# Optimization experiments

Measured on AMD Instinct MI355X. Metric: run time of the kernel, lower is better.

## Reference

```python
import jax, jax.numpy as jnp
import numpy as np
import math

RADIUS = 0.2
NSAMPLE = 32
M = 8
EPS = 1e-6

def _normalize(v, axis):
    n = jnp.sqrt(jnp.sum(v * v, axis=axis, keepdims=True))
    return v / (n + EPS)

def _ball_query(xyz, new_xyz, fps_idx):
    # Emulates pointnet2 ball_query: first NSAMPLE in-radius indices in scan
    # order, padded with the first found index; rows with no hits stay 0.
    B, N, _ = xyz.shape
    d2 = jnp.sum((new_xyz[:, :, None, :] - xyz[:, None, :, :]) ** 2, axis=-1)  # (B,P,N)
    mask = d2 < RADIUS * RADIUS
    keys = jnp.where(mask, jnp.arange(N, dtype=jnp.int32)[None, None, :], N)
    neg_top, _ = jax.lax.top_k(-keys, NSAMPLE)
    sorted_idx = -neg_top  # ascending first NSAMPLE in-radius indices (or N pads)
    cnt = jnp.sum(mask, axis=-1, keepdims=True)
    first = jnp.where(cnt > 0, jnp.minimum(sorted_idx[..., :1], N - 1), 0)
    j = jnp.arange(NSAMPLE)[None, None, :]
    idx = jnp.where(j < cnt, sorted_idx, first).astype(jnp.int32)
    return jnp.concatenate([fps_idx[:, :, None].astype(jnp.int32), idx], axis=-1)  # (B,P,S+1)

def _group(features, idx):
    # features (B,C,N), idx (B,P,S) -> (B,C,P,S)
    return jax.vmap(lambda f, i: f[:, i])(features, idx)

def _project_one(p):
    # reference vector in plane orthogonal to normalized p; p (B,3,P,1)
    p = _normalize(p, 1)
    px, py, pz = p[:, 0], p[:, 1], p[:, 2]
    colin = jnp.abs(px) > 1.0 - 1e-3
    rx = jnp.where(colin, -py * px, 1.0 - px * px)
    ry = jnp.where(colin, 1.0 - py * py, -px * py)
    rz = jnp.where(colin, -py * pz, -px * pz)
    return _normalize(jnp.stack([rx, ry, rz], axis=1), 1)

def _rot_sort(p, pts):
    # sort pts (B,3,P,S) along S by clockwise angle of projection onto plane orthogonal to p
    p = _normalize(p, 1)
    ref = _project_one(p)
    vert = jnp.sum(p * pts, axis=1, keepdims=True) * p
    projs = _normalize(pts - vert, 1)
    refb = jnp.broadcast_to(ref, projs.shape)
    sinus = jnp.sum(jnp.cross(refb, projs, axis=1) * p, axis=1, keepdims=True)
    cosinus = jnp.sum(refb * projs, axis=1, keepdims=True)
    angles = jnp.arctan2(sinus, cosinus)  # (B,1,P,S)
    close = jnp.sum(projs * projs, axis=1, keepdims=True) < 1e-12
    rnd = (jax.random.uniform(jax.random.key(42), angles.shape) - 0.5) * (2.0 * math.pi)
    angles = jnp.where(close, rnd, angles)
    ind = jnp.argsort(angles, axis=-1)
    return jnp.take_along_axis(pts, jnp.broadcast_to(ind, pts.shape), axis=-1)

def _calc_invariance(center, rel):
    norm2 = jnp.sqrt(jnp.sum(rel * rel, axis=1, keepdims=True) + 1e-12)
    c = _normalize(center, 1)
    cosang = jnp.sum(c * rel, axis=1, keepdims=True) / norm2
    angle = jnp.arccos(jnp.clip(cosang, -1.0 + EPS, 1.0 - EPS))
    return jnp.concatenate([norm2, angle], axis=1)  # (B,2,P,S)

def _to_quat(xyz):
    dist = jnp.sqrt(jnp.sum(xyz * xyz, axis=1, keepdims=True))
    ori = xyz / (dist + EPS)
    theta = dist / RADIUS * (math.pi / 2.0)
    return jnp.concatenate([jnp.cos(theta), jnp.sin(theta) * ori], axis=1)  # (B,4,P,S)

def _forward(xyz, new_xyz, fps_idx):
    idx = _ball_query(xyz, new_xyz, fps_idx)                 # (B,P,S+1)
    grouped = _group(jnp.swapaxes(xyz, 1, 2), idx)           # (B,3,P,S+1)
    centers = jnp.swapaxes(new_xyz, 1, 2)[..., None]         # (B,3,P,1)
    grouped = _rot_sort(centers, grouped[..., 1:] - centers) # (B,3,P,S)
    inv = _calc_invariance(centers, grouped)                 # (B,2,P,S)
    q = _to_quat(grouped)                                    # (B,4,P,S)
    quats = jnp.stack([jnp.roll(q, -m, axis=-1) for m in range(M)], axis=2)  # (B,4,M,P,S)
    B, _, _, P, S = quats.shape
    quats = quats.reshape(B, 4 * M, P, S)
    return jnp.concatenate([inv, quats], axis=1)             # (B,34,P,S)

def setup_inputs() -> dict:
    key = jax.random.key(0)
    k1, k2 = jax.random.split(key)
    B, N, P = 4, 8192, 2048
    xyz = jax.random.uniform(k1, (B, N, 3), dtype=jnp.float32)
    fps_idx = jax.random.randint(k2, (B, P), 0, N, dtype=jnp.int32)
    new_xyz = jax.vmap(lambda x, i: x[i])(xyz, fps_idx)
    return {"xyz": xyz, "new_xyz": new_xyz, "fps_idx": fps_idx}

def reference(xyz, new_xyz, fps_idx):
    return _forward(xyz, new_xyz, fps_idx)
```

## Files before the change

### kernel.cpp

```cpp
#include <hip/hip_runtime.h>
#include <math.h>

constexpr int Bc  = 4;
constexpr int Nc  = 8192;
constexpr int Pc  = 2048;
constexpr int Sc  = 32;
constexpr int CHc = 34;
constexpr int WSTRIDE = 40;
constexpr int NQ  = Bc * Pc;
constexpr int SOA_OFF = NQ * WSTRIDE;
constexpr int BN      = Bc * Nc;

#define THREEFRY_PARTITIONABLE 1

#define FMUL __fmul_rn
#define FADD __fadd_rn
#define FSUB __fsub_rn

__device__ __forceinline__ unsigned tf_rotl(unsigned x, int r) {
  return (x << r) | (x >> (32 - r));
}

__device__ __forceinline__ void threefry2x32_k42(unsigned& x0, unsigned& x1) {
  const unsigned ks0 = 0u, ks1 = 42u, ks2 = 0u ^ 42u ^ 0x1BD11BDAu;
  x0 += ks0; x1 += ks1;
#define TF_ROUND(r) { x0 += x1; x1 = tf_rotl(x1, (r)); x1 ^= x0; }
  TF_ROUND(13) TF_ROUND(15) TF_ROUND(26) TF_ROUND(6)
  x0 += ks1; x1 += ks2 + 1u;
  TF_ROUND(17) TF_ROUND(29) TF_ROUND(16) TF_ROUND(24)
  x0 += ks2; x1 += ks0 + 2u;
  TF_ROUND(13) TF_ROUND(15) TF_ROUND(26) TF_ROUND(6)
  x0 += ks0; x1 += ks1 + 3u;
  TF_ROUND(17) TF_ROUND(29) TF_ROUND(16) TF_ROUND(24)
  x0 += ks1; x1 += ks2 + 4u;
  TF_ROUND(13) TF_ROUND(15) TF_ROUND(26) TF_ROUND(6)
  x0 += ks2; x1 += ks0 + 5u;
#undef TF_ROUND
}

__device__ __forceinline__ float jax_rnd_angle(unsigned n) {
#if THREEFRY_PARTITIONABLE
  unsigned x0 = 0u, x1 = n;
  threefry2x32_k42(x0, x1);
  unsigned bits = x0 ^ x1;
#else
  const unsigned half = (unsigned)(Bc * Pc * Sc) / 2u;
  unsigned x0, x1;
  bool second = (n >= half);
  if (second) { x0 = n - half; x1 = n; } else { x0 = n; x1 = n + half; }
  threefry2x32_k42(x0, x1);
  unsigned bits = second ? x1 : x0;
#endif
  float u = __uint_as_float((bits >> 9) | 0x3F800000u) - 1.0f;
  return FMUL(FSUB(u, 0.5f), (float)(2.0 * 3.141592653589793));
}

__device__ __forceinline__ float dot3rn(float ax, float ay, float az,
                                        float bx, float by, float bz) {
  return FADD(FADD(FMUL(ax, bx), FMUL(ay, by)), FMUL(az, bz));
}

__global__ __launch_bounds__(256)
void soa_kernel(const float* __restrict__ xyz, float* __restrict__ wsf)
{
  const int i = blockIdx.x * 256 + threadIdx.x;
  if (i < BN) {
    wsf[SOA_OFF + 0 * BN + i] = xyz[i * 3 + 0];
    wsf[SOA_OFF + 1 * BN + i] = xyz[i * 3 + 1];
    wsf[SOA_OFF + 2 * BN + i] = xyz[i * 3 + 2];
  }
}

__global__ __launch_bounds__(256)
void ball_kernel(const float* __restrict__ wsf,
                 const float* __restrict__ new_xyz,
                 int* __restrict__ ws)
{
  const int wave = threadIdx.x >> 6;
  const int lane = threadIdx.x & 63;
  const int q    = blockIdx.x * 4 + wave;
  const int b    = q >> 11;
  const int p    = q & 2047;

  const float* sxb = wsf + SOA_OFF + 0 * BN + b * Nc;
  const float* syb = wsf + SOA_OFF + 1 * BN + b * Nc;
  const float* szb = wsf + SOA_OFF + 2 * BN + b * Nc;

  const float cx = new_xyz[((size_t)b * Pc + p) * 3 + 0];
  const float cy = new_xyz[((size_t)b * Pc + p) * 3 + 1];
  const float cz = new_xyz[((size_t)b * Pc + p) * 3 + 2];

  int* wq = ws + (size_t)q * WSTRIDE;
  const float R2 = (float)(0.2 * 0.2);
  const unsigned long long below = (1ull << lane) - 1ull;

  auto loadw = [&](int basew, float xs[8], float ys[8], float zs[8]) {
    #pragma unroll
    for (int k = 0; k < 8; ++k) {
      const int i = basew + k * 64 + lane;
      xs[k] = sxb[i];
      ys[k] = syb[i];
      zs[k] = szb[i];
    }
  };
  auto procw = [&](int basew, const float xs[8], const float ys[8],
                   const float zs[8], int& run) {
    #pragma unroll
    for (int k = 0; k < 8; ++k) {
      const float dx = FSUB(cx, xs[k]);
      const float dy = FSUB(cy, ys[k]);
      const float dz = FSUB(cz, zs[k]);
      const float d2 = FADD(FADD(FMUL(dx, dx), FMUL(dy, dy)), FMUL(dz, dz));
      const bool m = d2 < R2;
      const unsigned long long mask = __ballot(m);
      if (m) {
        const int pos = run + (int)__popcll(mask & below);
        if (pos < Sc) wq[pos] = basew + k * 64 + lane;
      }
      run += (int)__popcll(mask);
    }
  };

  float ax[8], ay[8], az[8], bx[8], by[8], bz[8];
  loadw(0, ax, ay, az);
  int run = 0;
  #pragma unroll 1
  for (int basew = 0; basew < Nc; basew += 1024) {
    loadw(basew + 512, bx, by, bz);
    procw(basew, ax, ay, az, run);
    if (run >= Sc) break;
    loadw((basew + 1024) & (Nc - 1), ax, ay, az);
    procw(basew + 512, bx, by, bz, run);
    if (run >= Sc) break;
  }
  if (lane == 0) wq[Sc] = (run > Sc) ? Sc : run;
}

__global__ __launch_bounds__(256)
void emit_kernel(const float* __restrict__ xyz,
                 const float* __restrict__ new_xyz,
                 const int* __restrict__ ws,
                 float* __restrict__ out)
{
  const int wave = threadIdx.x >> 6;
  const int lane = threadIdx.x & 63;
  const int half = lane >> 5;
  const int hofs = half << 5;
  const int j    = lane & 31;
  const int q    = blockIdx.x * 8 + wave * 2 + half;
  const int b    = q >> 11;
  const int p    = q & 2047;

  const float* xb = xyz + (size_t)b * Nc * 3;
  const float cx = new_xyz[((size_t)b * Pc + p) * 3 + 0];
  const float cy = new_xyz[((size_t)b * Pc + p) * 3 + 1];
  const float cz = new_xyz[((size_t)b * Pc + p) * 3 + 2];

  const int* wq = ws + (size_t)q * WSTRIDE;
  const int cnt = wq[Sc];

  const int gi = wq[(j < cnt) ? j : 0];

  const float ptx = xb[gi * 3 + 0];
  const float pty = xb[gi * 3 + 1];
  const float ptz = xb[gi * 3 + 2];
  const float relx = FSUB(ptx, cx);
  const float rely = FSUB(pty, cy);
  const float relz = FSUB(ptz, cz);

  const float n1  = __fsqrt_rn(dot3rn(cx, cy, cz, cx, cy, cz));
  const float id1 = FADD(n1, 1e-6f);
  const float p1x = __fdiv_rn(cx, id1);
  const float p1y = __fdiv_rn(cy, id1);
  const float p1z = __fdiv_rn(cz, id1);

  const float n2  = __fsqrt_rn(dot3rn(p1x, p1y, p1z, p1x, p1y, p1z));
  const float id2 = FADD(n2, 1e-6f);
  const float p2x = __fdiv_rn(p1x, id2);
  const float p2y = __fdiv_rn(p1y, id2);
  const float p2z = __fdiv_rn(p1z, id2);

  const bool colin = fabsf(p2x) > (float)(1.0 - 0.001);
  const float rxv = colin ? FMUL(-p2y, p2x) : FSUB(1.0f, FMUL(p2x, p2x));
  const float ryv = colin ? FSUB(1.0f, FMUL(p2y, p2y)) : FMUL(-p2x, p2y);
  const float rzv = colin ? FMUL(-p2y, p2z) : FMUL(-p2x, p2z);
  const float nr  = __fsqrt_rn(dot3rn(rxv, ryv, rzv, rxv, ryv, rzv));
  const float idr = FADD(nr, 1e-6f);
  const float refx = __fdiv_rn(rxv, idr);
  const float refy = __fdiv_rn(ryv, idr);
  const float refz = __fdiv_rn(rzv, idr);

  const float sdot = dot3rn(p1x, p1y, p1z, relx, rely, relz);
  const float wx = FSUB(relx, FMUL(sdot, p1x));
  const float wy = FSUB(rely, FMUL(sdot, p1y));
  const float wz = FSUB(relz, FMUL(sdot, p1z));
  const float nw  = __fsqrt_rn(dot3rn(wx, wy, wz, wx, wy, wz));
  const float idw = FADD(nw, 1e-6f);
  const float prx = __fdiv_rn(wx, idw);
  const float pry = __fdiv_rn(wy, idw);
  const float prz = __fdiv_rn(wz, idw);

  const float s2 = dot3rn(prx, pry, prz, prx, pry, prz);

  float angle;
  if (s2 < 1e-12f) {
    const unsigned n = ((unsigned)q << 5) | (unsigned)j;
    angle = jax_rnd_angle(n);
  } else {
    const float ccx = FSUB(FMUL(refy, prz), FMUL(refz, pry));
    const float ccy = FSUB(FMUL(refz, prx), FMUL(refx, prz));
    const float ccz = FSUB(FMUL(refx, pry), FMUL(refy, prx));
    const float sinus   = dot3rn(ccx, ccy, ccz, p1x, p1y, p1z);
    const float cosinus = dot3rn(refx, refy, refz, prx, pry, prz);
    angle = atan2f(sinus, cosinus);
  }

  const unsigned ab   = __float_as_uint(angle);
  const unsigned skey = (ab & 0x80000000u) ? ~ab : (ab | 0x80000000u);
  unsigned long long key = ((unsigned long long)skey << 32) | (unsigned)j;

  #pragma unroll
  for (int k = 2; k <= 32; k <<= 1) {
    #pragma unroll
    for (int jj = k >> 1; jj > 0; jj >>= 1) {
      const unsigned long long other = __shfl_xor(key, jj);
      const bool up      = ((j & k) == 0);
      const bool lower   = ((j & jj) == 0);
      const bool takeMin = (lower == up);
      const unsigned long long mn = (key < other) ? key : other;
      const unsigned long long mx = (key < other) ? other : key;
      key = takeMin ? mn : mx;
    }
  }
  const int oj = (int)(key & 31u);

  const float sx = __shfl(relx, oj + hofs);
  const float sy = __shfl(rely, oj + hofs);
  const float sz = __shfl(relz, oj + hofs);

  const float dotr  = sx * sx + sy * sy + sz * sz;
  const float norm2 = sqrtf(dotr + 1e-12f);
  float cosang = (p1x * sx + p1y * sy + p1z * sz) / norm2;
  const float CL = (float)(1.0 - 1e-6);
  cosang = fminf(fmaxf(cosang, -CL), CL);
  const float ainv = acosf(cosang);

  const float dist = sqrtf(dotr);
  const float invd = 1.0f / (dist + 1e-6f);
  const float oxv = sx * invd, oyv = sy * invd, ozv = sz * invd;
  const float theta = (dist / 0.2f) * (float)(3.141592653589793 / 2.0);
  float st, ct;
  sincosf(theta, &st, &ct);
  const float qw = ct, qx = st * oxv, qy = st * oyv, qz = st * ozv;

  const size_t chs   = (size_t)Pc * Sc;
  const size_t baseo = (size_t)b * CHc * chs + (size_t)p * Sc + (size_t)j;

  out[baseo + 0 * chs] = norm2;
  out[baseo + 1 * chs] = ainv;
  #pragma unroll
  for (int m = 0; m < 8; ++m) {
    const int src = ((j + m) & 31) + hofs;
    const float vw = __shfl(qw, src);
    const float vx = __shfl(qx, src);
    const float vy = __shfl(qy, src);
    const float vz = __shfl(qz, src);
    out[baseo + (size_t)(2 + 0 * 8 + m) * chs] = vw;
    out[baseo + (size_t)(2 + 1 * 8 + m) * chs] = vx;
    out[baseo + (size_t)(2 + 2 * 8 + m) * chs] = vy;
    out[baseo + (size_t)(2 + 3 * 8 + m) * chs] = vz;
  }
}

extern "C" void kernel_launch(void* const* d_in, const int* in_sizes, int n_in,
                              void* d_out, int out_size, void* d_ws, size_t ws_size,
                              hipStream_t stream) {
  const float* xyz     = (const float*)d_in[0];
  const float* new_xyz = (const float*)d_in[1];
  float* out = (float*)d_out;
  int*   ws  = (int*)d_ws;
  float* wsf = (float*)d_ws;

  hipLaunchKernelGGL(soa_kernel, dim3((BN + 255) / 256), dim3(256), 0, stream,
                     xyz, wsf);

  hipLaunchKernelGGL(ball_kernel, dim3(NQ / 4), dim3(256), 0, stream,
                     wsf, new_xyz, ws);

  hipLaunchKernelGGL(emit_kernel, dim3(NQ / 8), dim3(256), 0, stream,
                     xyz, new_xyz, ws, out);
}
```

Measured before the change: 87.04 us.

## Share LDS-staged point windows across 16 queries per block in ball query

The ball-query kernel now has each block handle 16 query centers (4 per wave). Point coordinates are staged cooperatively into double-buffered LDS windows of 512 points, so each point load is reused across four centers per wave and sixteen per block. Hit indices are gathered in LDS and written out at the end, and the block exits early only when all waves are done. This cuts global/L2 traffic per query, but adds a block-wide barrier per window, and a block can now keep scanning past the point where a single query would have stopped.

Result: slower. 109.5 us (+25.8%).

```diff
diff --git a/kernel.cpp b/kernel.cpp
--- a/kernel.cpp
+++ b/kernel.cpp
@@ -10,6 +10,7 @@
 constexpr int NQ  = Bc * Pc;
 constexpr int SOA_OFF = NQ * WSTRIDE;
 constexpr int BN      = Bc * Nc;
+constexpr int NWIN    = Nc / 512;
 
 #define THREEFRY_PARTITIONABLE 1
 
@@ -76,64 +77,94 @@
                  const float* __restrict__ new_xyz,
                  int* __restrict__ ws)
 {
-  const int wave = threadIdx.x >> 6;
-  const int lane = threadIdx.x & 63;
-  const int q    = blockIdx.x * 4 + wave;
-  const int b    = q >> 11;
-  const int p    = q & 2047;
+  __shared__ float sx[2][512], sy[2][512], sz[2][512];
+  __shared__ int   sIdxL[16][Sc];
+  __shared__ int   sdone[4];
+
+  const int tid  = threadIdx.x;
+  const int wave = tid >> 6;
+  const int lane = tid & 63;
+  const int q0    = blockIdx.x * 16;
+  const int qbase = q0 + wave * 4;
+  const int b     = q0 >> 11;
 
   const float* sxb = wsf + SOA_OFF + 0 * BN + b * Nc;
   const float* syb = wsf + SOA_OFF + 1 * BN + b * Nc;
   const float* szb = wsf + SOA_OFF + 2 * BN + b * Nc;
 
-  const float cx = new_xyz[((size_t)b * Pc + p) * 3 + 0];
-  const float cy = new_xyz[((size_t)b * Pc + p) * 3 + 1];
-  const float cz = new_xyz[((size_t)b * Pc + p) * 3 + 2];
-
-  int* wq = ws + (size_t)q * WSTRIDE;
+  float cx[4], cy[4], cz[4];
+  #pragma unroll
+  for (int i = 0; i < 4; ++i) {
+    const int p = (qbase + i) & 2047;
+    cx[i] = new_xyz[((size_t)b * Pc + p) * 3 + 0];
+    cy[i] = new_xyz[((size_t)b * Pc + p) * 3 + 1];
+    cz[i] = new_xyz[((size_t)b * Pc + p) * 3 + 2];
+  }
+
   const float R2 = (float)(0.2 * 0.2);
   const unsigned long long below = (1ull << lane) - 1ull;
 
-  auto loadw = [&](int basew, float xs[8], float ys[8], float zs[8]) {
-    #pragma unroll
-    for (int k = 0; k < 8; ++k) {
-      const int i = basew + k * 64 + lane;
-      xs[k] = sxb[i];
-      ys[k] = syb[i];
-      zs[k] = szb[i];
+  auto stage = [&](int wnd, int buf) {
+    const int basep = wnd * 512;
+    sx[buf][tid]       = sxb[basep + tid];
+    sy[buf][tid]       = syb[basep + tid];
+    sz[buf][tid]       = szb[basep + tid];
+    sx[buf][tid + 256] = sxb[basep + tid + 256];
+    sy[buf][tid + 256] = syb[basep + tid + 256];
+    sz[buf][tid + 256] = szb[basep + tid + 256];
+  };
+
+  int run4[4] = {0, 0, 0, 0};
+
+  auto procwin = [&](int wnd, int buf) {
+    #pragma unroll 1
+    for (int g = 0; g < 8; ++g) {
+      const float px = sx[buf][g * 64 + lane];
+      const float py = sy[buf][g * 64 + lane];
+      const float pz = sz[buf][g * 64 + lane];
+      #pragma unroll
+      for (int i = 0; i < 4; ++i) {
+        const float dx = FSUB(cx[i], px);
+        const float dy = FSUB(cy[i], py);
+        const float dz = FSUB(cz[i], pz);
+        const float d2 = FADD(FADD(FMUL(dx, dx), FMUL(dy, dy)), FMUL(dz, dz));
+        const bool m = d2 < R2;
+        const unsigned long long mask = __ballot(m);
+        if (m) {
+          const int pos = run4[i] + (int)__popcll(mask & below);
+          if (pos < Sc) sIdxL[wave * 4 + i][pos] = wnd * 512 + g * 64 + lane;
+        }
+        run4[i] += (int)__popcll(mask);
+      }
     }
   };
-  auto procw = [&](int basew, const float xs[8], const float ys[8],
-                   const float zs[8], int& run) {
-    #pragma unroll
-    for (int k = 0; k < 8; ++k) {
-      const float dx = FSUB(cx, xs[k]);
-      const float dy = FSUB(cy, ys[k]);
-      const float dz = FSUB(cz, zs[k]);
-      const float d2 = FADD(FADD(FMUL(dx, dx), FMUL(dy, dy)), FMUL(dz, dz));
-      const bool m = d2 < R2;
-      const unsigned long long mask = __ballot(m);
-      if (m) {
-        const int pos = run + (int)__popcll(mask & below);
-        if (pos < Sc) wq[pos] = basew + k * 64 + lane;
-      }
-      run += (int)__popcll(mask);
+
+  if (tid < 4) sdone[tid] = 0;
+  stage(0, 0);
+  bool mydone = false;
+  int w = 0;
+  #pragma unroll 1
+  for (;;) {
+    __syncthreads();
+    if (w >= NWIN) break;
+    if ((sdone[0] & sdone[1] & sdone[2] & sdone[3]) != 0) break;
+    if (w + 1 < NWIN) stage(w + 1, (w + 1) & 1);
+    if (!mydone) {
+      procwin(w, w & 1);
+      mydone = (run4[0] >= Sc) & (run4[1] >= Sc) &
+               (run4[2] >= Sc) & (run4[3] >= Sc);
+      if (mydone && lane == 0) sdone[wave] = 1;
     }
-  };
-
-  float ax[8], ay[8], az[8], bx[8], by[8], bz[8];
-  loadw(0, ax, ay, az);
-  int run = 0;
-  #pragma unroll 1
-  for (int basew = 0; basew < Nc; basew += 1024) {
-    loadw(basew + 512, bx, by, bz);
-    procw(basew, ax, ay, az, run);
-    if (run >= Sc) break;
-    loadw((basew + 1024) & (Nc - 1), ax, ay, az);
-    procw(basew + 512, bx, by, bz, run);
-    if (run >= Sc) break;
-  }
-  if (lane == 0) wq[Sc] = (run > Sc) ? Sc : run;
+    ++w;
+  }
+
+  #pragma unroll
+  for (int i = 0; i < 4; ++i) {
+    int* wq = ws + (size_t)(qbase + i) * WSTRIDE;
+    const int cnt = (run4[i] > Sc) ? Sc : run4[i];
+    if (lane < Sc) wq[lane] = sIdxL[wave * 4 + i][lane];
+    if (lane == 0) wq[Sc] = cnt;
+  }
 }
 
 __global__ __launch_bounds__(256)
@@ -284,7 +315,7 @@
   hipLaunchKernelGGL(soa_kernel, dim3((BN + 255) / 256), dim3(256), 0, stream,
                      xyz, wsf);
 
-  hipLaunchKernelGGL(ball_kernel, dim3(NQ / 4), dim3(256), 0, stream,
+  hipLaunchKernelGGL(ball_kernel, dim3(NQ / 16), dim3(256), 0, stream,
                      wsf, new_xyz, ws);
 
   hipLaunchKernelGGL(emit_kernel, dim3(NQ / 8), dim3(256), 0, stream,
```

## Fuse SoA transpose, ball query and emit into one kernel with two queries per wave

Applied to the files above, without the earlier changes.

Merges the three kernels into one: each wave now handles two query centers, scanning the point cloud once and testing both against each loaded point. Neighbor indices go to LDS instead of a global workspace, and points are read directly from the AoS xyz array, so the SoA transpose kernel is dropped. This removes two launches and the workspace round-trip and halves the number of point loads per query. In exchange each wave keeps scanning until both queries are full, loads become strided AoS reads, and the scan and emit phases now share one block's occupancy.

New measurement: 84.50 us. -2.9%, faster.

```diff
diff --git a/kernel.cpp b/kernel.cpp
--- a/kernel.cpp
+++ b/kernel.cpp
@@ -1,15 +1,13 @@
 #include <hip/hip_runtime.h>
 #include <math.h>
+
 
 constexpr int Bc  = 4;
 constexpr int Nc  = 8192;
 constexpr int Pc  = 2048;
 constexpr int Sc  = 32;
 constexpr int CHc = 34;
-constexpr int WSTRIDE = 40;
 constexpr int NQ  = Bc * Pc;
-constexpr int SOA_OFF = NQ * WSTRIDE;
-constexpr int BN      = Bc * Nc;
 
 #define THREEFRY_PARTITIONABLE 1
 
@@ -61,36 +59,27 @@
 }
 
 __global__ __launch_bounds__(256)
-void soa_kernel(const float* __restrict__ xyz, float* __restrict__ wsf)
+void qgq_fused(const float* __restrict__ xyz,
+               const float* __restrict__ new_xyz,
+               float* __restrict__ out)
 {
-  const int i = blockIdx.x * 256 + threadIdx.x;
-  if (i < BN) {
-    wsf[SOA_OFF + 0 * BN + i] = xyz[i * 3 + 0];
-    wsf[SOA_OFF + 1 * BN + i] = xyz[i * 3 + 1];
-    wsf[SOA_OFF + 2 * BN + i] = xyz[i * 3 + 2];
-  }
-}
-
-__global__ __launch_bounds__(256)
-void ball_kernel(const float* __restrict__ wsf,
-                 const float* __restrict__ new_xyz,
-                 int* __restrict__ ws)
-{
+  __shared__ int sIdx[4][2 * Sc];
+
   const int wave = threadIdx.x >> 6;
   const int lane = threadIdx.x & 63;
-  const int q    = blockIdx.x * 4 + wave;
-  const int b    = q >> 11;
-  const int p    = q & 2047;
-
-  const float* sxb = wsf + SOA_OFF + 0 * BN + b * Nc;
-  const float* syb = wsf + SOA_OFF + 1 * BN + b * Nc;
-  const float* szb = wsf + SOA_OFF + 2 * BN + b * Nc;
-
-  const float cx = new_xyz[((size_t)b * Pc + p) * 3 + 0];
-  const float cy = new_xyz[((size_t)b * Pc + p) * 3 + 1];
-  const float cz = new_xyz[((size_t)b * Pc + p) * 3 + 2];
-
-  int* wq = ws + (size_t)q * WSTRIDE;
+  const int q0   = blockIdx.x * 8 + wave * 2;
+  const int b    = q0 >> 11;
+  const int p0   = q0 & 2047;
+
+  const float* xb = xyz + (size_t)b * Nc * 3;
+  const float c0x = new_xyz[((size_t)b * Pc + p0) * 3 + 0];
+  const float c0y = new_xyz[((size_t)b * Pc + p0) * 3 + 1];
+  const float c0z = new_xyz[((size_t)b * Pc + p0) * 3 + 2];
+  const float c1x = new_xyz[((size_t)b * Pc + p0 + 1) * 3 + 0];
+  const float c1y = new_xyz[((size_t)b * Pc + p0 + 1) * 3 + 1];
+  const float c1z = new_xyz[((size_t)b * Pc + p0 + 1) * 3 + 2];
+
+  int* sw = sIdx[wave];
   const float R2 = (float)(0.2 * 0.2);
   const unsigned long long below = (1ull << lane) - 1ull;
 
@@ -98,68 +87,73 @@
     #pragma unroll
     for (int k = 0; k < 8; ++k) {
       const int i = basew + k * 64 + lane;
-      xs[k] = sxb[i];
-      ys[k] = syb[i];
-      zs[k] = szb[i];
+      xs[k] = xb[i * 3 + 0];
+      ys[k] = xb[i * 3 + 1];
+      zs[k] = xb[i * 3 + 2];
     }
   };
+
+  int run0 = 0, run1 = 0;
   auto procw = [&](int basew, const float xs[8], const float ys[8],
-                   const float zs[8], int& run) {
+                   const float zs[8]) {
     #pragma unroll
     for (int k = 0; k < 8; ++k) {
-      const float dx = FSUB(cx, xs[k]);
-      const float dy = FSUB(cy, ys[k]);
-      const float dz = FSUB(cz, zs[k]);
-      const float d2 = FADD(FADD(FMUL(dx, dx), FMUL(dy, dy)), FMUL(dz, dz));
-      const bool m = d2 < R2;
-      const unsigned long long mask = __ballot(m);
-      if (m) {
-        const int pos = run + (int)__popcll(mask & below);
-        if (pos < Sc) wq[pos] = basew + k * 64 + lane;
+      const int idx = basew + k * 64 + lane;
+      {
+        const float dx = FSUB(c0x, xs[k]);
+        const float dy = FSUB(c0y, ys[k]);
+        const float dz = FSUB(c0z, zs[k]);
+        const float d2 = FADD(FADD(FMUL(dx, dx), FMUL(dy, dy)), FMUL(dz, dz));
+        const bool m = d2 < R2;
+        const unsigned long long mask = __ballot(m);
+        if (m) {
+          const int pos = run0 + (int)__popcll(mask & below);
+          if (pos < Sc) sw[pos] = idx;
+        }
+        run0 += (int)__popcll(mask);
       }
-      run += (int)__popcll(mask);
+      {
+        const float dx = FSUB(c1x, xs[k]);
+        const float dy = FSUB(c1y, ys[k]);
+        const float dz = FSUB(c1z, zs[k]);
+        const float d2 = FADD(FADD(FMUL(dx, dx), FMUL(dy, dy)), FMUL(dz, dz));
+        const bool m = d2 < R2;
+        const unsigned long long mask = __ballot(m);
+        if (m) {
+          const int pos = run1 + (int)__popcll(mask & below);
+          if (pos < Sc) sw[Sc + pos] = idx;
+        }
+        run1 += (int)__popcll(mask);
+      }
     }
   };
 
   float ax[8], ay[8], az[8], bx[8], by[8], bz[8];
   loadw(0, ax, ay, az);
-  int run = 0;
   #pragma unroll 1
   for (int basew = 0; basew < Nc; basew += 1024) {
     loadw(basew + 512, bx, by, bz);
-    procw(basew, ax, ay, az, run);
-    if (run >= Sc) break;
+    procw(basew, ax, ay, az);
+    if (run0 >= Sc && run1 >= Sc) break;
     loadw((basew + 1024) & (Nc - 1), ax, ay, az);
-    procw(basew + 512, bx, by, bz, run);
-    if (run >= Sc) break;
-  }
-  if (lane == 0) wq[Sc] = (run > Sc) ? Sc : run;
-}
-
-__global__ __launch_bounds__(256)
-void emit_kernel(const float* __restrict__ xyz,
-                 const float* __restrict__ new_xyz,
-                 const int* __restrict__ ws,
-                 float* __restrict__ out)
-{
-  const int wave = threadIdx.x >> 6;
-  const int lane = threadIdx.x & 63;
+    procw(basew + 512, bx, by, bz);
+    if (run0 >= Sc && run1 >= Sc) break;
+  }
+
   const int half = lane >> 5;
   const int hofs = half << 5;
   const int j    = lane & 31;
-  const int q    = blockIdx.x * 8 + wave * 2 + half;
-  const int b    = q >> 11;
+  const int q    = q0 + half;
   const int p    = q & 2047;
 
-  const float* xb = xyz + (size_t)b * Nc * 3;
-  const float cx = new_xyz[((size_t)b * Pc + p) * 3 + 0];
-  const float cy = new_xyz[((size_t)b * Pc + p) * 3 + 1];
-  const float cz = new_xyz[((size_t)b * Pc + p) * 3 + 2];
-
-  const int* wq = ws + (size_t)q * WSTRIDE;
-  const int cnt = wq[Sc];
-
-  const int gi = wq[(j < cnt) ? j : 0];
+  const int c0c = (run0 > Sc) ? Sc : run0;
+  const int c1c = (run1 > Sc) ? Sc : run1;
+  const int cnt = half ? c1c : c0c;
+  const float cx = half ? c1x : c0x;
+  const float cy = half ? c1y : c0y;
+  const float cz = half ? c1z : c0z;
+
+  const int gi = sw[hofs + ((j < cnt) ? j : 0)];
 
   const float ptx = xb[gi * 3 + 0];
   const float pty = xb[gi * 3 + 1];
@@ -278,15 +272,7 @@
   const float* xyz     = (const float*)d_in[0];
   const float* new_xyz = (const float*)d_in[1];
   float* out = (float*)d_out;
-  int*   ws  = (int*)d_ws;
-  float* wsf = (float*)d_ws;
-
-  hipLaunchKernelGGL(soa_kernel, dim3((BN + 255) / 256), dim3(256), 0, stream,
-                     xyz, wsf);
-
-  hipLaunchKernelGGL(ball_kernel, dim3(NQ / 4), dim3(256), 0, stream,
-                     wsf, new_xyz, ws);
-
-  hipLaunchKernelGGL(emit_kernel, dim3(NQ / 8), dim3(256), 0, stream,
-                     xyz, new_xyz, ws, out);
-}
+
+  hipLaunchKernelGGL(qgq_fused, dim3(NQ / 8), dim3(256), 0, stream,
+                     xyz, new_xyz, out);
+}
```
